# Kernel tuning notes

Hardware: AMD Instinct MI355X
Metric: run time of the kernel (lower is better)

The kernel has to match this reference:

```python
import jax, jax.numpy as jnp
import numpy as np

BN_EPS = 1e-5


def setup_inputs() -> dict:
    key = jax.random.key(0)
    ks = jax.random.split(key, 5)
    b, c, h, w = 4, 128, 64, 64
    x = jax.random.normal(ks[0], (b, c, h, w), dtype=jnp.float32)
    # conv1x1 c -> 2c (fan-in scaled)
    w_inp = jax.random.normal(ks[1], (2 * c, c), dtype=jnp.float32) / np.sqrt(c)
    b_inp = jax.random.normal(ks[2], (2 * c,), dtype=jnp.float32) * 0.01
    bn_gamma = jnp.ones((2 * c,), dtype=jnp.float32)
    bn_beta = jnp.zeros((2 * c,), dtype=jnp.float32)
    bn_mean = jnp.zeros((2 * c,), dtype=jnp.float32)
    bn_var = jnp.ones((2 * c,), dtype=jnp.float32)
    w_out = jax.random.normal(ks[3], (c, c), dtype=jnp.float32) / np.sqrt(c)
    b_out = jax.random.normal(ks[4], (c,), dtype=jnp.float32) * 0.01
    return {
        "x": x, "w_inp": w_inp, "b_inp": b_inp,
        "bn_gamma": bn_gamma, "bn_beta": bn_beta,
        "bn_mean": bn_mean, "bn_var": bn_var,
        "w_out": w_out, "b_out": b_out,
    }


def reference(x, w_inp, b_inp, bn_gamma, bn_beta, bn_mean, bn_var, w_out, b_out):
    b, c, h, w = x.shape
    scale = c ** (-0.5)
    # project_inp: conv1x1 (c -> 2c) + BatchNorm2d (eval mode, running stats)
    t = jnp.einsum('bchw,oc->bohw', x, w_inp) + b_inp[None, :, None, None]
    bn_scale = bn_gamma * jax.lax.rsqrt(bn_var + BN_EPS)
    t = t * bn_scale[None, :, None, None] + (bn_beta - bn_mean * bn_scale)[None, :, None, None]
    # split qv along channels, flatten spatial to tokens: [b, N, c], N = h*w
    q = t[:, :c].reshape(b, c, h * w).transpose(0, 2, 1)
    v = t[:, c:].reshape(b, c, h * w).transpose(0, 2, 1)
    # self-similarity attention on q: [b, N, N]
    atn = jax.nn.softmax(jnp.einsum('bnc,bmc->bnm', q, q) * scale, axis=-1)
    y = jnp.einsum('bnm,bmc->bnc', atn, v)  # [b, N, c]
    y = y.transpose(0, 2, 1).reshape(b, c, h, w)
    # project_out: conv1x1 c -> c
    y = jnp.einsum('bchw,oc->bohw', y, w_out) + b_out[None, :, None, None]
    return (y, atn)
```

## Files before the change

kernel.cpp:

```cpp
#include <hip/hip_runtime.h>
#include <stdint.h>
#include <math.h>

#define C_DIM 128
#define N_TOK 4096
#define NB 4
#define LOG2E 1.4426950408889634f

typedef __attribute__((ext_vector_type(8))) short bf16x8;
typedef __attribute__((ext_vector_type(4))) float f32x4;

__device__ __forceinline__ unsigned short f2bf(float f) {
  unsigned u = __builtin_bit_cast(unsigned, f);
  unsigned r = (u + 0x7FFFu + ((u >> 16) & 1u)) >> 16;
  return (unsigned short)r;
}
__device__ __forceinline__ float bf2f(unsigned short h) {
  return __builtin_bit_cast(float, ((unsigned)h) << 16);
}
__device__ __forceinline__ void gload_lds16(const void* g, void* l) {
  __builtin_amdgcn_global_load_lds((const __attribute__((address_space(1))) void*)g,
                                   (__attribute__((address_space(3))) void*)l,
                                   16, 0, 0);
}

__global__ __launch_bounds__(256) void proj_in_kernel(
    const float* __restrict__ x, const float* __restrict__ w_inp,
    const float* __restrict__ b_inp, const float* __restrict__ gamma,
    const float* __restrict__ beta, const float* __restrict__ mean,
    const float* __restrict__ var,
    unsigned short* __restrict__ q, unsigned short* __restrict__ vT) {
  __shared__ char smem[35840];
  unsigned short* xh = (unsigned short*)smem;
  unsigned short* xl = (unsigned short*)(smem + 17408);

  const int tid = threadIdx.x;
  const int b = blockIdx.x >> 6;
  const int n0 = (blockIdx.x & 63) << 6;
  const int lane = tid & 63;
  const int wave = tid >> 6;
  const int l15 = lane & 15, lg = lane >> 4;

  {
    const int c = tid >> 1;
    const int j0 = (tid & 1) * 32;
    const float* src = x + ((size_t)b * C_DIM + c) * N_TOK + n0 + j0;
#pragma unroll
    for (int j = 0; j < 32; j += 4) {
      float4 v4 = *(const float4*)(src + j);
#pragma unroll
      for (int e = 0; e < 4; e++) {
        float f = (&v4.x)[e];
        unsigned short hi = f2bf(f);
        unsigned short lo = f2bf(f - bf2f(hi));
        int n = j0 + j + e;
        xh[n * 136 + c] = hi;
        xl[n * 136 + c] = lo;
      }
    }
  }
  __syncthreads();

  f32x4 acc[4][4];
#pragma unroll
  for (int i = 0; i < 4; i++)
#pragma unroll
    for (int j = 0; j < 4; j++) acc[i][j] = {0.f, 0.f, 0.f, 0.f};

#pragma unroll
  for (int ks = 0; ks < 4; ks++) {
    bf16x8 ah[4], al[4];
#pragma unroll
    for (int ot = 0; ot < 4; ot++) {
      const int o = wave * 64 + ot * 16 + l15;
      const float* wp = w_inp + o * C_DIM + ks * 32 + lg * 8;
      float4 w0 = *(const float4*)wp;
      float4 w1 = *(const float4*)(wp + 4);
#pragma unroll
      for (int e = 0; e < 8; e++) {
        float f = (e < 4) ? (&w0.x)[e] : (&w1.x)[e - 4];
        unsigned short hi = f2bf(f);
        ah[ot][e] = (short)hi;
        al[ot][e] = (short)f2bf(f - bf2f(hi));
      }
    }
#pragma unroll
    for (int nt = 0; nt < 4; nt++) {
      const int off = (nt * 16 + l15) * 136 + ks * 32 + lg * 8;
      bf16x8 bh = *(const bf16x8*)(xh + off);
      bf16x8 bl = *(const bf16x8*)(xl + off);
#pragma unroll
      for (int ot = 0; ot < 4; ot++) {
        acc[ot][nt] = __builtin_amdgcn_mfma_f32_16x16x32_bf16(ah[ot], bh, acc[ot][nt], 0, 0, 0);
        acc[ot][nt] = __builtin_amdgcn_mfma_f32_16x16x32_bf16(ah[ot], bl, acc[ot][nt], 0, 0, 0);
        acc[ot][nt] = __builtin_amdgcn_mfma_f32_16x16x32_bf16(al[ot], bh, acc[ot][nt], 0, 0, 0);
      }
    }
  }
  __syncthreads();

  unsigned short* qT = (unsigned short*)smem;
  unsigned short* vTl = (unsigned short*)(smem + 17408);

#pragma unroll
  for (int ot = 0; ot < 4; ot++) {
#pragma unroll
    for (int r = 0; r < 4; r++) {
      const int o = wave * 64 + ot * 16 + lg * 4 + r;
      float A = gamma[o] * rsqrtf(var[o] + 1e-5f);
      float Bo = beta[o] + (b_inp[o] - mean[o]) * A;
#pragma unroll
      for (int nt = 0; nt < 4; nt++) {
        float val = acc[ot][nt][r] * A + Bo;
        unsigned short hv = f2bf(val);
        int n = nt * 16 + l15;
        if (wave < 2) {
          qT[n * 136 + o] = hv;
        } else {
          vTl[(o - 128) * 72 + n] = hv;
        }
      }
    }
  }
  __syncthreads();
  {
    int j = tid >> 2, c0 = (tid & 3) * 32;
    unsigned short* dst = q + ((size_t)b * N_TOK + n0 + j) * C_DIM + c0;
    const unsigned short* s = qT + j * 136 + c0;
#pragma unroll
    for (int i = 0; i < 32; i += 8) *(bf16x8*)(dst + i) = *(const bf16x8*)(s + i);
  }
  {
    int c = tid >> 1, h = (tid & 1) * 32;
    unsigned short* dst = vT + ((size_t)b * C_DIM + c) * N_TOK + n0 + h;
    const unsigned short* s = vTl + c * 72 + h;
#pragma unroll
    for (int i = 0; i < 32; i += 8) *(bf16x8*)(dst + i) = *(const bf16x8*)(s + i);
  }
}

__global__ __launch_bounds__(256) void attn_kernel(
    const unsigned short* __restrict__ q, const unsigned short* __restrict__ vT,
    const float* __restrict__ w_out, const float* __restrict__ b_out,
    float* __restrict__ yout, float* __restrict__ atn) {
  __shared__ char smem[74752];

  const int tid = threadIdx.x;
  const int lane = tid & 63;
  const int wave = tid >> 6;
  const int l15 = lane & 15, lg = lane >> 4, l7 = lane & 7;
  const int b = blockIdx.x >> 6;
  const int q0 = (blockIdx.x & 63) << 6;
  const int row0 = q0 + wave * 16;

  const unsigned short* qb = q + (size_t)b * N_TOK * C_DIM;
  const unsigned short* vb = vT + (size_t)b * C_DIM * N_TOK;

  bf16x8 qf[4];
#pragma unroll
  for (int ks = 0; ks < 4; ks++)
    qf[ks] = *(const bf16x8*)(qb + (size_t)(row0 + l15) * C_DIM + ks * 32 + lg * 8);

  int koff[4];
#pragma unroll
  for (int ks = 0; ks < 4; ks++) koff[ks] = (ks * 64 + lg * 16) ^ (l7 * 16);
  const int krow = l15 * 256;
  const int vrow = l15 * 128;

  auto stageK = [&](int kt, int buf) {
    char* base = smem + buf * 16384;
#pragma unroll
    for (int i = 0; i < 4; i++) {
      int lin = i * 256 + tid;
      int key = lin >> 4;
      int c = ((lin & 15) * 8) ^ ((key & 7) * 8);
      gload_lds16(qb + (size_t)(kt * 64 + key) * C_DIM + c, base + lin * 16);
    }
  };
  auto stageV = [&](int kt, int buf) {
    char* base = smem + 32768 + buf * 16384;
#pragma unroll
    for (int i = 0; i < 4; i++) {
      int lin = i * 256 + tid;
      int c = lin >> 3;
      int key = ((lin & 7) * 8) ^ ((c & 7) * 8);
      gload_lds16(vb + (size_t)c * N_TOK + kt * 64 + key, base + lin * 16);
    }
  };

  const float scale = 0.08838834764831845f;
  float m[4], l[4];
#pragma unroll
  for (int r = 0; r < 4; r++) { m[r] = -1e30f; l[r] = 0.f; }

  stageK(0, 0);
  __syncthreads();
  for (int kt = 0; kt < 64; kt++) {
    if (kt + 1 < 64) stageK(kt + 1, (kt + 1) & 1);
    const char* kb = smem + (kt & 1) * 16384;
    float s_all[4][4];
#pragma unroll
    for (int nt = 0; nt < 4; nt++) {
      f32x4 acc = {0.f, 0.f, 0.f, 0.f};
#pragma unroll
      for (int ks = 0; ks < 4; ks++) {
        bf16x8 bk = *(const bf16x8*)(kb + nt * 4096 + krow + koff[ks]);
        acc = __builtin_amdgcn_mfma_f32_16x16x32_bf16(qf[ks], bk, acc, 0, 0, 0);
      }
#pragma unroll
      for (int r = 0; r < 4; r++) s_all[nt][r] = acc[r] * scale;
    }
#pragma unroll
    for (int r = 0; r < 4; r++) {
      float mx = fmaxf(fmaxf(s_all[0][r], s_all[1][r]), fmaxf(s_all[2][r], s_all[3][r]));
      mx = fmaxf(mx, __shfl_xor(mx, 1));
      mx = fmaxf(mx, __shfl_xor(mx, 2));
      mx = fmaxf(mx, __shfl_xor(mx, 4));
      mx = fmaxf(mx, __shfl_xor(mx, 8));
      float mn = fmaxf(m[r], mx);
      float sum = 0.f;
#pragma unroll
      for (int nt = 0; nt < 4; nt++) sum += exp2f((s_all[nt][r] - mn) * LOG2E);
      sum += __shfl_xor(sum, 1);
      sum += __shfl_xor(sum, 2);
      sum += __shfl_xor(sum, 4);
      sum += __shfl_xor(sum, 8);
      l[r] = l[r] * exp2f((m[r] - mn) * LOG2E) + sum;
      m[r] = mn;
    }
    __syncthreads();
  }

  float invl[4];
#pragma unroll
  for (int r = 0; r < 4; r++) invl[r] = 1.0f / l[r];

  f32x4 yacc[8];
#pragma unroll
  for (int ct = 0; ct < 8; ct++) yacc[ct] = {0.f, 0.f, 0.f, 0.f};

  stageK(0, 0);
  stageV(0, 0);
  __syncthreads();
  unsigned short* pb = (unsigned short*)(smem + 65536 + wave * 2304);
  float* atnb = atn + ((size_t)b * N_TOK + row0) * N_TOK;

  for (int kt = 0; kt < 64; kt++) {
    if (kt + 1 < 64) { stageK(kt + 1, (kt + 1) & 1); stageV(kt + 1, (kt + 1) & 1); }
    const char* kb = smem + (kt & 1) * 16384;
    const char* vbf = smem + 32768 + (kt & 1) * 16384;
#pragma unroll
    for (int nt = 0; nt < 4; nt++) {
      f32x4 acc = {0.f, 0.f, 0.f, 0.f};
#pragma unroll
      for (int ks = 0; ks < 4; ks++) {
        bf16x8 bk = *(const bf16x8*)(kb + nt * 4096 + krow + koff[ks]);
        acc = __builtin_amdgcn_mfma_f32_16x16x32_bf16(qf[ks], bk, acc, 0, 0, 0);
      }
#pragma unroll
      for (int r = 0; r < 4; r++) {
        float p = exp2f((acc[r] * scale - m[r]) * LOG2E) * invl[r];
        atnb[(size_t)(lg * 4 + r) * N_TOK + kt * 64 + nt * 16 + l15] = p;
        pb[(lg * 4 + r) * 72 + nt * 16 + l15] = (unsigned short)f2bf(p);
      }
    }
#pragma unroll
    for (int ks2 = 0; ks2 < 2; ks2++) {
      bf16x8 ap = *(const bf16x8*)(pb + l15 * 72 + ks2 * 32 + lg * 8);
#pragma unroll
      for (int ct = 0; ct < 8; ct++) {
        bf16x8 bv = *(const bf16x8*)(vbf + ct * 2048 + vrow + koff[ks2]);
        yacc[ct] = __builtin_amdgcn_mfma_f32_16x16x32_bf16(ap, bv, yacc[ct], 0, 0, 0);
      }
    }
    __syncthreads();
  }

  __syncthreads();
  unsigned short* yl = (unsigned short*)(smem + wave * 16384);
  float* ol = (float*)(smem + wave * 16384 + 4608);
#pragma unroll
  for (int ct = 0; ct < 8; ct++)
#pragma unroll
    for (int r = 0; r < 4; r++)
      yl[(lg * 4 + r) * 136 + ct * 16 + l15] = f2bf(yacc[ct][r]);

  bf16x8 af[4];
#pragma unroll
  for (int ks = 0; ks < 4; ks++)
    af[ks] = *(const bf16x8*)(yl + l15 * 136 + ks * 32 + lg * 8);

#pragma unroll
  for (int cot = 0; cot < 8; cot++) {
    f32x4 oacc = {0.f, 0.f, 0.f, 0.f};
#pragma unroll
    for (int ks = 0; ks < 4; ks++) {
      const float* wp = w_out + (cot * 16 + l15) * C_DIM + ks * 32 + lg * 8;
      float4 w0 = *(const float4*)wp;
      float4 w1 = *(const float4*)(wp + 4);
      bf16x8 bw;
#pragma unroll
      for (int e = 0; e < 8; e++) bw[e] = (short)f2bf((e < 4) ? (&w0.x)[e] : (&w1.x)[e - 4]);
      oacc = __builtin_amdgcn_mfma_f32_16x16x32_bf16(af[ks], bw, oacc, 0, 0, 0);
    }
    float bo = b_out[cot * 16 + l15];
#pragma unroll
    for (int r = 0; r < 4; r++) ol[(cot * 16 + l15) * 20 + lg * 4 + r] = oacc[r] + bo;
  }
#pragma unroll
  for (int i = 0; i < 2; i++) {
    int co = i * 64 + lane;
    float* dst = yout + ((size_t)b * C_DIM + co) * N_TOK + row0;
    const float* s = ol + co * 20;
#pragma unroll
    for (int jj = 0; jj < 16; jj += 4) *(float4*)(dst + jj) = *(const float4*)(s + jj);
  }
}

extern "C" void kernel_launch(void* const* d_in, const int* in_sizes, int n_in,
                              void* d_out, int out_size, void* d_ws, size_t ws_size,
                              hipStream_t stream) {
  const float* x = (const float*)d_in[0];
  const float* w_inp = (const float*)d_in[1];
  const float* b_inp = (const float*)d_in[2];
  const float* gamma = (const float*)d_in[3];
  const float* beta = (const float*)d_in[4];
  const float* mean = (const float*)d_in[5];
  const float* var = (const float*)d_in[6];
  const float* w_out = (const float*)d_in[7];
  const float* b_out = (const float*)d_in[8];

  float* out = (float*)d_out;
  float* yout = out;
  float* atn = out + (size_t)NB * C_DIM * N_TOK;

  unsigned short* q = (unsigned short*)d_ws;
  unsigned short* vT = q + (size_t)NB * N_TOK * C_DIM;

  proj_in_kernel<<<256, 256, 0, stream>>>(x, w_inp, b_inp, gamma, beta, mean, var, q, vT);
  attn_kernel<<<256, 256, 0, stream>>>(q, vT, w_out, b_out, yout, atn);
}
```

Baseline: 214.6 us.

## Split key tiles across wave pairs and double the attention grid

Each block now handles 32 query rows instead of 64, and each pair of waves splits every 64-key tile into two 32-key halves. Partial softmax statistics are merged through shared memory, and the partial PV accumulators are summed before the output projection. The grid grows from 256 to 512 blocks, which should fill the MI355X's CUs better. In exchange, each K/V tile is loaded from global memory twice as often per query row, and the merge adds extra syncs and shared-memory traffic.

```diff
diff --git a/kernel.cpp b/kernel.cpp
--- a/kernel.cpp
+++ b/kernel.cpp
@@ -143,15 +143,17 @@
     const unsigned short* __restrict__ q, const unsigned short* __restrict__ vT,
     const float* __restrict__ w_out, const float* __restrict__ b_out,
     float* __restrict__ yout, float* __restrict__ atn) {
-  __shared__ char smem[74752];
+  __shared__ char smem[71168];
 
   const int tid = threadIdx.x;
   const int lane = tid & 63;
   const int wave = tid >> 6;
+  const int rg = wave >> 1;
+  const int kh = wave & 1;
   const int l15 = lane & 15, lg = lane >> 4, l7 = lane & 7;
-  const int b = blockIdx.x >> 6;
-  const int q0 = (blockIdx.x & 63) << 6;
-  const int row0 = q0 + wave * 16;
+  const int b = blockIdx.x >> 7;
+  const int q0 = (blockIdx.x & 127) << 5;
+  const int row0 = q0 + rg * 16;
 
   const unsigned short* qb = q + (size_t)b * N_TOK * C_DIM;
   const unsigned short* vb = vT + (size_t)b * C_DIM * N_TOK;
@@ -164,6 +166,7 @@
   int koff[4];
 #pragma unroll
   for (int ks = 0; ks < 4; ks++) koff[ks] = (ks * 64 + lg * 16) ^ (l7 * 16);
+  const int koff2 = (kh * 64 + lg * 16) ^ (l7 * 16);
   const int krow = l15 * 256;
   const int vrow = l15 * 128;
 
@@ -189,7 +192,7 @@
   };
 
   const float scale = 0.08838834764831845f;
-  float m[4], l[4];
+  float m[4], l[4], invl[4];
 #pragma unroll
   for (int r = 0; r < 4; r++) { m[r] = -1e30f; l[r] = 0.f; }
 
@@ -198,9 +201,10 @@
   for (int kt = 0; kt < 64; kt++) {
     if (kt + 1 < 64) stageK(kt + 1, (kt + 1) & 1);
     const char* kb = smem + (kt & 1) * 16384;
-    float s_all[4][4];
-#pragma unroll
-    for (int nt = 0; nt < 4; nt++) {
+    float s_all[2][4];
+#pragma unroll
+    for (int nt16 = 0; nt16 < 2; nt16++) {
+      const int nt = kh * 2 + nt16;
       f32x4 acc = {0.f, 0.f, 0.f, 0.f};
 #pragma unroll
       for (int ks = 0; ks < 4; ks++) {
@@ -208,19 +212,17 @@
         acc = __builtin_amdgcn_mfma_f32_16x16x32_bf16(qf[ks], bk, acc, 0, 0, 0);
       }
 #pragma unroll
-      for (int r = 0; r < 4; r++) s_all[nt][r] = acc[r] * scale;
+      for (int r = 0; r < 4; r++) s_all[nt16][r] = acc[r] * scale;
     }
 #pragma unroll
     for (int r = 0; r < 4; r++) {
-      float mx = fmaxf(fmaxf(s_all[0][r], s_all[1][r]), fmaxf(s_all[2][r], s_all[3][r]));
+      float mx = fmaxf(s_all[0][r], s_all[1][r]);
       mx = fmaxf(mx, __shfl_xor(mx, 1));
       mx = fmaxf(mx, __shfl_xor(mx, 2));
       mx = fmaxf(mx, __shfl_xor(mx, 4));
       mx = fmaxf(mx, __shfl_xor(mx, 8));
       float mn = fmaxf(m[r], mx);
-      float sum = 0.f;
-#pragma unroll
-      for (int nt = 0; nt < 4; nt++) sum += exp2f((s_all[nt][r] - mn) * LOG2E);
+      float sum = exp2f((s_all[0][r] - mn) * LOG2E) + exp2f((s_all[1][r] - mn) * LOG2E);
       sum += __shfl_xor(sum, 1);
       sum += __shfl_xor(sum, 2);
       sum += __shfl_xor(sum, 4);
@@ -231,9 +233,27 @@
     __syncthreads();
   }
 
-  float invl[4];
-#pragma unroll
-  for (int r = 0; r < 4; r++) invl[r] = 1.0f / l[r];
+  float* statsL = (float*)(smem + 70656);
+  if (l15 == 0) {
+#pragma unroll
+    for (int r = 0; r < 4; r++) {
+      float* p = statsL + (((kh * 2 + rg) * 16) + lg * 4 + r) * 2;
+      p[0] = m[r];
+      p[1] = l[r];
+    }
+  }
+  __syncthreads();
+#pragma unroll
+  for (int r = 0; r < 4; r++) {
+    const int row = lg * 4 + r;
+    const float* p0 = statsL + ((rg * 16) + row) * 2;
+    const float* p1 = statsL + (((2 + rg) * 16) + row) * 2;
+    float m0 = p0[0], l0 = p0[1], m1 = p1[0], l1 = p1[1];
+    float M = fmaxf(m0, m1);
+    float L = l0 * exp2f((m0 - M) * LOG2E) + l1 * exp2f((m1 - M) * LOG2E);
+    m[r] = M;
+    invl[r] = 1.0f / L;
+  }
 
   f32x4 yacc[8];
 #pragma unroll
@@ -242,7 +262,7 @@
   stageK(0, 0);
   stageV(0, 0);
   __syncthreads();
-  unsigned short* pb = (unsigned short*)(smem + 65536 + wave * 2304);
+  unsigned short* pb = (unsigned short*)(smem + 65536 + wave * 1280);
   float* atnb = atn + ((size_t)b * N_TOK + row0) * N_TOK;
 
   for (int kt = 0; kt < 64; kt++) {
@@ -250,7 +270,8 @@
     const char* kb = smem + (kt & 1) * 16384;
     const char* vbf = smem + 32768 + (kt & 1) * 16384;
 #pragma unroll
-    for (int nt = 0; nt < 4; nt++) {
+    for (int nt16 = 0; nt16 < 2; nt16++) {
+      const int nt = kh * 2 + nt16;
       f32x4 acc = {0.f, 0.f, 0.f, 0.f};
 #pragma unroll
       for (int ks = 0; ks < 4; ks++) {
@@ -260,60 +281,75 @@
 #pragma unroll
       for (int r = 0; r < 4; r++) {
         float p = exp2f((acc[r] * scale - m[r]) * LOG2E) * invl[r];
-        atnb[(size_t)(lg * 4 + r) * N_TOK + kt * 64 + nt * 16 + l15] = p;
-        pb[(lg * 4 + r) * 72 + nt * 16 + l15] = (unsigned short)f2bf(p);
-      }
-    }
-#pragma unroll
-    for (int ks2 = 0; ks2 < 2; ks2++) {
-      bf16x8 ap = *(const bf16x8*)(pb + l15 * 72 + ks2 * 32 + lg * 8);
+        atnb[(size_t)(lg * 4 + r) * N_TOK + kt * 64 + kh * 32 + nt16 * 16 + l15] = p;
+        pb[(lg * 4 + r) * 40 + nt16 * 16 + l15] = (unsigned short)f2bf(p);
+      }
+    }
+    {
+      bf16x8 ap = *(const bf16x8*)(pb + l15 * 40 + lg * 8);
 #pragma unroll
       for (int ct = 0; ct < 8; ct++) {
-        bf16x8 bv = *(const bf16x8*)(vbf + ct * 2048 + vrow + koff[ks2]);
+        bf16x8 bv = *(const bf16x8*)(vbf + ct * 2048 + vrow + koff2);
         yacc[ct] = __builtin_amdgcn_mfma_f32_16x16x32_bf16(ap, bv, yacc[ct], 0, 0, 0);
       }
     }
     __syncthreads();
   }
 
-  __syncthreads();
-  unsigned short* yl = (unsigned short*)(smem + wave * 16384);
-  float* ol = (float*)(smem + wave * 16384 + 4608);
-#pragma unroll
-  for (int ct = 0; ct < 8; ct++)
-#pragma unroll
-    for (int r = 0; r < 4; r++)
-      yl[(lg * 4 + r) * 136 + ct * 16 + l15] = f2bf(yacc[ct][r]);
-
-  bf16x8 af[4];
-#pragma unroll
-  for (int ks = 0; ks < 4; ks++)
-    af[ks] = *(const bf16x8*)(yl + l15 * 136 + ks * 32 + lg * 8);
-
-#pragma unroll
-  for (int cot = 0; cot < 8; cot++) {
-    f32x4 oacc = {0.f, 0.f, 0.f, 0.f};
-#pragma unroll
-    for (int ks = 0; ks < 4; ks++) {
-      const float* wp = w_out + (cot * 16 + l15) * C_DIM + ks * 32 + lg * 8;
-      float4 w0 = *(const float4*)wp;
-      float4 w1 = *(const float4*)(wp + 4);
-      bf16x8 bw;
-#pragma unroll
-      for (int e = 0; e < 8; e++) bw[e] = (short)f2bf((e < 4) ? (&w0.x)[e] : (&w1.x)[e - 4]);
-      oacc = __builtin_amdgcn_mfma_f32_16x16x32_bf16(af[ks], bw, oacc, 0, 0, 0);
-    }
-    float bo = b_out[cot * 16 + l15];
-#pragma unroll
-    for (int r = 0; r < 4; r++) ol[(cot * 16 + l15) * 20 + lg * 4 + r] = oacc[r] + bo;
-  }
-#pragma unroll
-  for (int i = 0; i < 2; i++) {
-    int co = i * 64 + lane;
-    float* dst = yout + ((size_t)b * C_DIM + co) * N_TOK + row0;
-    const float* s = ol + co * 20;
-#pragma unroll
-    for (int jj = 0; jj < 16; jj += 4) *(float4*)(dst + jj) = *(const float4*)(s + jj);
+  float* ymergeF = (float*)(smem + 32768);
+  if (kh) {
+#pragma unroll
+    for (int ct = 0; ct < 8; ct++)
+#pragma unroll
+      for (int r = 0; r < 4; r++)
+        ymergeF[(rg * 16 + lg * 4 + r) * 136 + ct * 16 + l15] = yacc[ct][r];
+  }
+  __syncthreads();
+  if (!kh) {
+#pragma unroll
+    for (int ct = 0; ct < 8; ct++)
+#pragma unroll
+      for (int r = 0; r < 4; r++)
+        yacc[ct][r] += ymergeF[(rg * 16 + lg * 4 + r) * 136 + ct * 16 + l15];
+
+    unsigned short* yl = (unsigned short*)(smem + rg * 16384);
+    float* ol = (float*)(smem + rg * 16384 + 4608);
+#pragma unroll
+    for (int ct = 0; ct < 8; ct++)
+#pragma unroll
+      for (int r = 0; r < 4; r++)
+        yl[(lg * 4 + r) * 136 + ct * 16 + l15] = f2bf(yacc[ct][r]);
+
+    bf16x8 af[4];
+#pragma unroll
+    for (int ks = 0; ks < 4; ks++)
+      af[ks] = *(const bf16x8*)(yl + l15 * 136 + ks * 32 + lg * 8);
+
+#pragma unroll
+    for (int cot = 0; cot < 8; cot++) {
+      f32x4 oacc = {0.f, 0.f, 0.f, 0.f};
+#pragma unroll
+      for (int ks = 0; ks < 4; ks++) {
+        const float* wp = w_out + (cot * 16 + l15) * C_DIM + ks * 32 + lg * 8;
+        float4 w0 = *(const float4*)wp;
+        float4 w1 = *(const float4*)(wp + 4);
+        bf16x8 bw;
+#pragma unroll
+        for (int e = 0; e < 8; e++) bw[e] = (short)f2bf((e < 4) ? (&w0.x)[e] : (&w1.x)[e - 4]);
+        oacc = __builtin_amdgcn_mfma_f32_16x16x32_bf16(af[ks], bw, oacc, 0, 0, 0);
+      }
+      float bo = b_out[cot * 16 + l15];
+#pragma unroll
+      for (int r = 0; r < 4; r++) ol[(cot * 16 + l15) * 20 + lg * 4 + r] = oacc[r] + bo;
+    }
+#pragma unroll
+    for (int i = 0; i < 2; i++) {
+      int co = i * 64 + lane;
+      float* dst = yout + ((size_t)b * C_DIM + co) * N_TOK + row0;
+      const float* s = ol + co * 20;
+#pragma unroll
+      for (int jj = 0; jj < 16; jj += 4) *(float4*)(dst + jj) = *(const float4*)(s + jj);
+    }
   }
 }
 
@@ -338,5 +374,5 @@
   unsigned short* vT = q + (size_t)NB * N_TOK * C_DIM;
 
   proj_in_kernel<<<256, 256, 0, stream>>>(x, w_inp, b_inp, gamma, beta, mean, var, q, vT);
-  attn_kernel<<<256, 256, 0, stream>>>(q, vT, w_out, b_out, yout, atn);
-}
+  attn_kernel<<<512, 256, 0, stream>>>(q, vT, w_out, b_out, yout, atn);
+}
```

After: 212.8 us. Within noise of the previous version (-0.8%).
